# Performance work log

Measured on AMD Instinct MI355X. Metric: run time of the kernel, lower is better.

Reference implementation:

```python
import jax, jax.numpy as jnp
import numpy as np

S = 128          # spatial grid size per axis
N = 100000       # active voxels
C_IN = 32
C_OUT = 32
FS = 3           # filter size per axis -> 27 offsets


def _build_rulebook():
    """Build submanifold-conv rulebook: for each active site and each of the
    27 filter offsets, the index of the active neighbor (or masked out)."""
    rng = np.random.default_rng(0)
    coords = rng.integers(0, S, size=(2 * N, 3))
    lin = coords[:, 0] * S * S + coords[:, 1] * S + coords[:, 2]
    lin = np.unique(lin)[:N]                      # sorted unique active sites
    xyz = np.stack([lin // (S * S), (lin // S) % S, lin % S], axis=1)  # [N,3]
    offs = np.stack(np.meshgrid(*([np.arange(FS) - FS // 2] * 3), indexing='ij'), -1).reshape(-1, 3)  # [27,3]
    nb = xyz[:, None, :] + offs[None, :, :]       # [N,27,3]
    inb = np.all((nb >= 0) & (nb < S), axis=-1)   # in-bounds
    nb_lin = nb[..., 0] * S * S + nb[..., 1] * S + nb[..., 2]
    pos = np.searchsorted(lin, nb_lin)
    pos_c = np.clip(pos, 0, N - 1)
    found = inb & (lin[pos_c] == nb_lin)
    nbr_idx = np.where(found, pos_c, 0).astype(np.int32)   # [N,27]
    return nbr_idx, found


def setup_inputs() -> dict:
    key = jax.random.key(0)
    k1, k2 = jax.random.split(key)
    nbr_idx, nbr_mask = _build_rulebook()
    K = FS ** 3
    std = (2.0 / C_IN / K) ** 0.5   # matches module init
    return {
        'features': jax.random.normal(k1, (N, C_IN), dtype=jnp.float32),
        'weight': std * jax.random.normal(k2, (K, C_IN, C_OUT), dtype=jnp.float32),
        'bias': jnp.zeros((C_OUT,), dtype=jnp.float32),
        'nbr_idx': jnp.asarray(nbr_idx),
        'nbr_mask': jnp.asarray(nbr_mask),
    }


def reference(features, weight, bias, nbr_idx, nbr_mask):
    # Submanifold sparse conv: gather active neighbors per filter offset,
    # multiply by per-offset [Cin,Cout] weight, accumulate at active sites.
    gathered = jnp.where(nbr_mask[:, :, None], features[nbr_idx], 0.0)  # [N,K,Cin]
    out = jnp.einsum('nki,kio->no', gathered, weight) + bias            # [N,Cout]
    return out
```

## Files before the change

### kernel.cpp

```cpp
#include <hip/hip_runtime.h>
#include <hip/hip_bf16.h>

#define NVOX 100000
#define CIN 32
#define COUT 32
#define KOFF 27

typedef __attribute__((ext_vector_type(8))) short short8;
typedef __attribute__((ext_vector_type(4))) float float4v;
typedef __attribute__((ext_vector_type(4))) int   int4v;

__device__ __forceinline__ short f2bf(float x) {
    union { float f; unsigned u; } v; v.f = x;
    unsigned u = v.u;
    u += 0x7FFFu + ((u >> 16) & 1u);
    return (short)(u >> 16);
}

__global__ __launch_bounds__(512, 4) void subm_conv_kernel(
    const float* __restrict__ feat,
    const float* __restrict__ weight,
    const float* __restrict__ bias,
    const int* __restrict__ nbr_idx,
    const int* __restrict__ nbr_mask,
    float* __restrict__ out)
{
    __shared__ short8 wlds[KOFF * 2 * 64];

    const int tid = threadIdx.x;

    for (int g = tid; g < KOFF * 2 * 64; g += 512) {
        int k   = g >> 7;
        int rem = g & 127;
        int t   = rem >> 6;
        int ln  = rem & 63;
        int co  = t * 16 + (ln & 15);
        int cib = (ln >> 4) * 8;
        const float* wp = weight + (k * CIN + cib) * COUT + co;
        short8 b;
#pragma unroll
        for (int j = 0; j < 8; ++j) b[j] = f2bf(wp[j * COUT]);
        wlds[g] = b;
    }
    __syncthreads();

    const int lane = tid & 63;
    const int wave = tid >> 6;
    const int m    = lane & 15;
    const int quad = lane >> 4;

    const int v0 = (blockIdx.x * 8 + wave) * 16;
    int v = v0 + m;
    if (v > NVOX - 1) v = NVOX - 1;
    const int base = v * KOFF;

    int enc[KOFF];
#pragma unroll
    for (int k = 0; k < KOFF; ++k) enc[k] = nbr_idx[base + k];
    int mok[KOFF];
#pragma unroll
    for (int k = 0; k < KOFF; ++k) mok[k] = nbr_mask[base + k];
#pragma unroll
    for (int k = 0; k < KOFF; ++k) enc[k] = mok[k] ? enc[k] : -1;

    float4v acc0 = {0.f, 0.f, 0.f, 0.f};
    float4v acc1 = {0.f, 0.f, 0.f, 0.f};

    const int cioff = quad * 8;

    float4v b0buf[4], b1buf[4];
#pragma unroll
    for (int k = 0; k < 4; ++k) {
        int row = enc[k] < 0 ? 0 : enc[k];
        const float4v* fr = (const float4v*)(feat + (size_t)row * CIN + cioff);
        b0buf[k] = fr[0];
        b1buf[k] = fr[1];
    }

#pragma unroll
    for (int k = 0; k < KOFF; ++k) {
        const int slot = k & 3;
        float4v f0 = b0buf[slot];
        float4v f1 = b1buf[slot];
        if (k + 4 < KOFF) {
            int row = enc[k + 4] < 0 ? 0 : enc[k + 4];
            const float4v* fr = (const float4v*)(feat + (size_t)row * CIN + cioff);
            b0buf[slot] = fr[0];
            b1buf[slot] = fr[1];
        }

        union { short8 s; int4v i; } a;
        a.s[0] = f2bf(f0.x); a.s[1] = f2bf(f0.y); a.s[2] = f2bf(f0.z); a.s[3] = f2bf(f0.w);
        a.s[4] = f2bf(f1.x); a.s[5] = f2bf(f1.y); a.s[6] = f2bf(f1.z); a.s[7] = f2bf(f1.w);
        int zmask = enc[k] >= 0 ? ~0 : 0;
        a.i &= int4v{zmask, zmask, zmask, zmask};

        short8 wb0 = wlds[k * 128 + lane];
        short8 wb1 = wlds[k * 128 + 64 + lane];
        acc0 = __builtin_amdgcn_mfma_f32_16x16x32_bf16(a.s, wb0, acc0, 0, 0, 0);
        acc1 = __builtin_amdgcn_mfma_f32_16x16x32_bf16(a.s, wb1, acc1, 0, 0, 0);
    }

    const float bs0 = bias[m];
    const float bs1 = bias[16 + m];
#pragma unroll
    for (int r = 0; r < 4; ++r) {
        int vv = v0 + quad * 4 + r;
        if (vv < NVOX) {
            out[(size_t)vv * COUT + m]      = acc0[r] + bs0;
            out[(size_t)vv * COUT + 16 + m] = acc1[r] + bs1;
        }
    }
}

extern "C" void kernel_launch(void* const* d_in, const int* in_sizes, int n_in,
                              void* d_out, int out_size, void* d_ws, size_t ws_size,
                              hipStream_t stream) {
    const float* feat = (const float*)d_in[0];
    const float* wgt  = (const float*)d_in[1];
    const float* bias = (const float*)d_in[2];
    const int*   nidx = (const int*)d_in[3];
    const int*   nmsk = (const int*)d_in[4];
    float*       out  = (float*)d_out;

    const int block = 512;
    const int grid  = (NVOX + 127) / 128;
    subm_conv_kernel<<<grid, block, 0, stream>>>(feat, wgt, bias, nidx, nmsk, out);
}
```

Baseline: 111.1 us.

## Pre-convert features and weights to bf16 in separate kernels before gather-MFMA

Adds a pre-pass kernel that converts all features to bf16 in workspace, and another that lays out the weights directly as bf16 MFMA fragments. The main kernel then gathers half-width rows, copies weight fragments into LDS without per-block conversion, and deepens the gather prefetch from 4 to 8 offsets. The aim is to halve the gather traffic and drop the repeated per-block conversion work, at the cost of two extra launches and a full extra read and write of the feature array.

```diff
diff --git a/kernel.cpp b/kernel.cpp
--- a/kernel.cpp
+++ b/kernel.cpp
@@ -17,9 +17,37 @@
     return (short)(u >> 16);
 }
 
+__global__ __launch_bounds__(256) void feat_cvt_kernel(
+    const float* __restrict__ feat, unsigned short* __restrict__ fbf)
+{
+    int i = (blockIdx.x * 256 + threadIdx.x) * 4;
+    if (i >= NVOX * CIN) return;
+    float4v f = *(const float4v*)(feat + i);
+    short s[4] = { f2bf(f.x), f2bf(f.y), f2bf(f.z), f2bf(f.w) };
+    *(ulonglong1*)(fbf + i) = *(ulonglong1*)s;
+}
+
+__global__ __launch_bounds__(256) void wgt_cvt_kernel(
+    const float* __restrict__ weight, short8* __restrict__ wfrag)
+{
+    int g = blockIdx.x * 256 + threadIdx.x;
+    if (g >= KOFF * 2 * 64) return;
+    int k   = g >> 7;
+    int rem = g & 127;
+    int t   = rem >> 6;
+    int ln  = rem & 63;
+    int co  = t * 16 + (ln & 15);
+    int cib = (ln >> 4) * 8;
+    const float* wp = weight + (k * CIN + cib) * COUT + co;
+    short8 b;
+#pragma unroll
+    for (int j = 0; j < 8; ++j) b[j] = f2bf(wp[j * COUT]);
+    wfrag[g] = b;
+}
+
 __global__ __launch_bounds__(512, 4) void subm_conv_kernel(
-    const float* __restrict__ feat,
-    const float* __restrict__ weight,
+    const unsigned short* __restrict__ fbf,
+    const short8* __restrict__ wfrag,
     const float* __restrict__ bias,
     const int* __restrict__ nbr_idx,
     const int* __restrict__ nbr_mask,
@@ -28,20 +56,7 @@
     __shared__ short8 wlds[KOFF * 2 * 64];
 
     const int tid = threadIdx.x;
-
-    for (int g = tid; g < KOFF * 2 * 64; g += 512) {
-        int k   = g >> 7;
-        int rem = g & 127;
-        int t   = rem >> 6;
-        int ln  = rem & 63;
-        int co  = t * 16 + (ln & 15);
-        int cib = (ln >> 4) * 8;
-        const float* wp = weight + (k * CIN + cib) * COUT + co;
-        short8 b;
-#pragma unroll
-        for (int j = 0; j < 8; ++j) b[j] = f2bf(wp[j * COUT]);
-        wlds[g] = b;
-    }
+    for (int g = tid; g < KOFF * 2 * 64; g += 512) wlds[g] = wfrag[g];
     __syncthreads();
 
     const int lane = tid & 63;
@@ -68,30 +83,22 @@
 
     const int cioff = quad * 8;
 
-    float4v b0buf[4], b1buf[4];
+    short8 abuf[8];
 #pragma unroll
-    for (int k = 0; k < 4; ++k) {
+    for (int k = 0; k < 8; ++k) {
         int row = enc[k] < 0 ? 0 : enc[k];
-        const float4v* fr = (const float4v*)(feat + (size_t)row * CIN + cioff);
-        b0buf[k] = fr[0];
-        b1buf[k] = fr[1];
+        abuf[k] = *(const short8*)(fbf + (size_t)row * CIN + cioff);
     }
 
 #pragma unroll
     for (int k = 0; k < KOFF; ++k) {
-        const int slot = k & 3;
-        float4v f0 = b0buf[slot];
-        float4v f1 = b1buf[slot];
-        if (k + 4 < KOFF) {
-            int row = enc[k + 4] < 0 ? 0 : enc[k + 4];
-            const float4v* fr = (const float4v*)(feat + (size_t)row * CIN + cioff);
-            b0buf[slot] = fr[0];
-            b1buf[slot] = fr[1];
+        const int slot = k & 7;
+        union { short8 s; int4v i; } a;
+        a.s = abuf[slot];
+        if (k + 8 < KOFF) {
+            int row = enc[k + 8] < 0 ? 0 : enc[k + 8];
+            abuf[slot] = *(const short8*)(fbf + (size_t)row * CIN + cioff);
         }
-
-        union { short8 s; int4v i; } a;
-        a.s[0] = f2bf(f0.x); a.s[1] = f2bf(f0.y); a.s[2] = f2bf(f0.z); a.s[3] = f2bf(f0.w);
-        a.s[4] = f2bf(f1.x); a.s[5] = f2bf(f1.y); a.s[6] = f2bf(f1.z); a.s[7] = f2bf(f1.w);
         int zmask = enc[k] >= 0 ? ~0 : 0;
         a.i &= int4v{zmask, zmask, zmask, zmask};
 
@@ -123,7 +130,13 @@
     const int*   nmsk = (const int*)d_in[4];
     float*       out  = (float*)d_out;
 
+    unsigned short* fbf   = (unsigned short*)d_ws;
+    short8*         wfrag = (short8*)((char*)d_ws + (size_t)NVOX * CIN * 2);
+
+    feat_cvt_kernel<<<(NVOX * CIN / 4 + 255) / 256, 256, 0, stream>>>(feat, fbf);
+    wgt_cvt_kernel<<<(KOFF * 2 * 64 + 255) / 256, 256, 0, stream>>>(wgt, wfrag);
+
     const int block = 512;
     const int grid  = (NVOX + 127) / 128;
-    subm_conv_kernel<<<grid, block, 0, stream>>>(feat, wgt, bias, nidx, nmsk, out);
+    subm_conv_kernel<<<grid, block, 0, stream>>>(fbf, wfrag, bias, nidx, nmsk, out);
 }
```

Result: faster. 104.2 us (-6.2%).
